# Optimization experiments

Hardware: AMD Instinct MI355X
Metric: run time of the kernel (lower is better)

The kernel has to match this reference:

```python
import jax, jax.numpy as jnp
import numpy as np

B, L, DIM = 4, 2048, 512
H, D = 8, 64
SCALE = D ** -0.5
NEG = -10000.0


def setup_inputs() -> dict:
    key = jax.random.key(0)
    ks = jax.random.split(key, 5)
    std = 1.0 / np.sqrt(DIM)
    return {
        "x": jax.random.normal(ks[0], (B, L, DIM), dtype=jnp.float32),
        "wq": jax.random.normal(ks[1], (H * D, DIM), dtype=jnp.float32) * std,
        "wk": jax.random.normal(ks[2], (H * D, DIM), dtype=jnp.float32) * std,
        "wv": jax.random.normal(ks[3], (H * D, DIM), dtype=jnp.float32) * std,
        "wo": jax.random.normal(ks[4], (DIM, H * D), dtype=jnp.float32) * std,
    }


def reference(x, wq, wk, wv, wo):
    b, l, _ = x.shape
    # projections (torch Linear: y = x @ W.T), split heads -> [b,h,l,d]
    q = (x @ wq.T).reshape(b, l, H, D).transpose(0, 2, 1, 3)
    k = (x @ wk.T).reshape(b, l, H, D).transpose(0, 2, 1, 3)
    v = (x @ wv.T).reshape(b, l, H, D).transpose(0, 2, 1, 3)
    scores = jnp.einsum("bhld,bhsd->bhls", q, k) * SCALE
    scores = jnp.nan_to_num(scores, nan=0.0, posinf=10000.0, neginf=NEG)
    diag = jnp.eye(l, dtype=bool)[None, None]  # [1,1,l,l]
    scores = jnp.where(diag, NEG, scores)
    attn = jax.nn.softmax(scores, axis=-1)
    attn = jnp.where(diag, 0.0, attn)
    attn = jnp.nan_to_num(attn, nan=0.0, posinf=0.0, neginf=0.0)
    out = jnp.einsum("bhls,bhsd->bhld", attn, v)
    out = out.transpose(0, 2, 1, 3).reshape(b, l, H * D)
    return out @ wo.T
```

## Files before the change

kernel.cpp:

```cpp
#include <hip/hip_runtime.h>
#include <hip/hip_bf16.h>


#define Bsz 4
#define Lsz 2048
#define DIMsz 512
#define Hsz 8
#define Dsz 64

typedef _Float16 f16;
typedef __attribute__((ext_vector_type(8))) _Float16 f16x8;
typedef __attribute__((ext_vector_type(4))) _Float16 f16x4;
typedef __attribute__((ext_vector_type(2))) __fp16 fp16x2;
typedef __attribute__((ext_vector_type(4))) float f32x4;
typedef __attribute__((ext_vector_type(16))) float f32x16;
typedef unsigned int u32;
typedef __attribute__((ext_vector_type(2))) unsigned int u32x2;

#if __has_builtin(__builtin_amdgcn_exp2f)
#define EXP2(x) __builtin_amdgcn_exp2f(x)
#else
#define EXP2(x) __expf(0.6931471805599453f * (x))
#endif

__device__ __forceinline__ u32 pack2(float a, float b) {
#if __has_builtin(__builtin_amdgcn_cvt_pkrtz)
    fp16x2 h = __builtin_amdgcn_cvt_pkrtz(a, b);
    return __builtin_bit_cast(u32, h);
#else
    fp16x2 h; h.x = (__fp16)a; h.y = (__fp16)b;
    return __builtin_bit_cast(u32, h);
#endif
}

#if __has_builtin(__builtin_amdgcn_permlane32_swap)
__device__ __forceinline__ void plswap(u32& a, u32& b) {
    u32x2 r = __builtin_amdgcn_permlane32_swap(a, b, false, false);
    a = r.x; b = r.y;
}
#else
__device__ __forceinline__ void plswap(u32& a, u32& b) {
    u32 sa = (u32)__shfl_xor((int)a, 32);
    u32 sb = (u32)__shfl_xor((int)b, 32);
    bool hi = (threadIdx.x & 32) != 0;
    u32 na = hi ? sb : a;
    u32 nb = hi ? b : sa;
    a = na; b = nb;
}
#endif

__device__ __forceinline__ void gl2lds16(const void* g, void* l) {
    __builtin_amdgcn_global_load_lds(
        (const __attribute__((address_space(1))) u32*)g,
        (__attribute__((address_space(3))) u32*)l, 16, 0, 0);
}

__global__ __launch_bounds__(256) void pack_f16(
    const float* __restrict__ x, const float* __restrict__ wq,
    const float* __restrict__ wk, const float* __restrict__ wv,
    const float* __restrict__ wo,
    f16* __restrict__ xh, f16* __restrict__ w3h, f16* __restrict__ woh)
{
    int bx = blockIdx.x, seg, blk;
    if (bx < 4096) { seg = 0; blk = bx; }
    else { seg = 1 + ((bx - 4096) >> 8); blk = (bx - 4096) & 255; }
    const float* s; f16* d; float sc = 1.0f;
    switch (seg) {
        case 0: s = x;  d = xh;            break;
        case 1: s = wq; d = w3h;           sc = 0.18033688011112042f; break;
        case 2: s = wk; d = w3h + 262144;  break;
        case 3: s = wv; d = w3h + 524288;  break;
        default: s = wo; d = woh;          break;
    }
    int i = (blk * 256 + threadIdx.x) * 4;
    float4 v = *(const float4*)(s + i);
    f16x4 o;
    o.x = (f16)(v.x * sc); o.y = (f16)(v.y * sc);
    o.z = (f16)(v.z * sc); o.w = (f16)(v.w * sc);
    *(f16x4*)(d + i) = o;
}

__global__ __launch_bounds__(256) void gemm_qkv_f16(
    const f16* __restrict__ A, const f16* __restrict__ B,
    f16* __restrict__ qh, f16* __restrict__ kh, f16* __restrict__ vth)
{
    __shared__ __align__(16) char smem[32768];
    f16* Ash = (f16*)smem;
    f16* Bsh = (f16*)(smem + 16384);

    const int tid = threadIdx.x;
    const int w = tid >> 6, lane = tid & 63;
    const int quad = lane >> 4, low = lane & 15;
    const int wm = w >> 1, wn = w & 1;
    const int m0 = blockIdx.y * 128, n0 = blockIdx.x * 128;

    f32x4 acc[4][4];
    #pragma unroll
    for (int i = 0; i < 4; i++)
        #pragma unroll
        for (int j = 0; j < 4; j++) acc[i][j] = (f32x4){0.f, 0.f, 0.f, 0.f};

    #pragma unroll 1
    for (int k0 = 0; k0 < DIMsz; k0 += 64) {
        __syncthreads();
        #pragma unroll
        for (int j = 0; j < 4; j++) {
            int t = j * 256 + tid;
            int r = t >> 3, g = t & 7;
            int gc = (g ^ (r & 7)) * 8;
            char* lb = (char*)Ash + (j * 256 + w * 64) * 16;
            gl2lds16(A + (size_t)(m0 + r) * DIMsz + k0 + gc, lb);
            char* lb2 = (char*)Bsh + (j * 256 + w * 64) * 16;
            gl2lds16(B + (size_t)(n0 + r) * DIMsz + k0 + gc, lb2);
        }
        __syncthreads();

        #pragma unroll
        for (int ks2 = 0; ks2 < 2; ks2++) {
            f16x8 af[4], bf[4];
            #pragma unroll
            for (int mt = 0; mt < 4; mt++) {
                int ar = wm * 64 + mt * 16 + low;
                int c = ks2 * 4 + quad;
                af[mt] = *(const f16x8*)&Ash[ar * 64 + ((c ^ (ar & 7)) << 3)];
            }
            #pragma unroll
            for (int nt = 0; nt < 4; nt++) {
                int br = wn * 64 + nt * 16 + low;
                int c = ks2 * 4 + quad;
                bf[nt] = *(const f16x8*)&Bsh[br * 64 + ((c ^ (br & 7)) << 3)];
            }
            #pragma unroll
            for (int mt = 0; mt < 4; mt++)
                #pragma unroll
                for (int nt = 0; nt < 4; nt++)
                    acc[mt][nt] = __builtin_amdgcn_mfma_f32_16x16x32_f16(
                        af[mt], bf[nt], acc[mt][nt], 0, 0, 0);
        }
    }

    const int proj = n0 >> 9;
    if (proj < 2) {
        f16* dst = (proj == 0) ? qh : kh;
        #pragma unroll
        for (int nt = 0; nt < 4; nt++) {
            int n = n0 + wn * 64 + nt * 16 + low;
            int c = n & 511, h = c >> 6, d = c & 63;
            #pragma unroll
            for (int mt = 0; mt < 4; mt++)
                #pragma unroll
                for (int r = 0; r < 4; r++) {
                    int m = m0 + wm * 64 + mt * 16 + quad * 4 + r;
                    int b_ = m >> 11, l = m & (Lsz - 1);
                    size_t bh = (size_t)(b_ * Hsz + h);
                    dst[(bh * Lsz + l) * Dsz + d] = (f16)acc[mt][nt][r];
                }
        }
    } else {
        const int hb = (n0 & 511) >> 6;
        f16* Tv = (f16*)smem;
        const int b_ = m0 >> 11, l0 = m0 & (Lsz - 1);
        #pragma unroll 1
        for (int hs = 0; hs < 2; hs++) {
            __syncthreads();
            if (wn == hs) {
                #pragma unroll
                for (int nt = 0; nt < 4; nt++) {
                    int d = nt * 16 + low;
                    #pragma unroll
                    for (int mt = 0; mt < 4; mt++)
                        #pragma unroll
                        for (int r = 0; r < 4; r++) {
                            int l = wm * 64 + mt * 16 + quad * 4 + r;
                            Tv[d * 136 + l] = (f16)acc[mt][nt][r];
                        }
                }
            }
            __syncthreads();
            int d = tid >> 2, seg = tid & 3;
            size_t bh = (size_t)(b_ * Hsz + hb + hs);
            f16* dstp = vth + (bh * 64 + d) * (size_t)Lsz + l0 + seg * 32;
            const f16* srcp = Tv + d * 136 + seg * 32;
            #pragma unroll
            for (int j = 0; j < 4; j++)
                *(f16x8*)(dstp + j * 8) = *(const f16x8*)(srcp + j * 8);
        }
    }
}

__global__ __launch_bounds__(256, 3) void attn_mfma(
    const f16* __restrict__ q, const f16* __restrict__ k,
    const f16* __restrict__ vt, f16* __restrict__ ctx)
{
    __shared__ __align__(16) char smem[32768];
    __shared__ float Ls[4][2][32];

    f16* Ks = (f16*)smem;
    f16* Vs = (f16*)(smem + 16384);

    const int tid = threadIdx.x;
    const int w = tid >> 6, lane = tid & 63;
    const int col = lane & 31;
    const int h = lane >> 5;
    const int bh = blockIdx.x;
    const int qb = blockIdx.y;
    const int q0 = qb * 64;
    const size_t kvb = (size_t)bh * Lsz;

    f16x8 qf[2][4];
    #pragma unroll
    for (int qt = 0; qt < 2; qt++)
        #pragma unroll
        for (int s = 0; s < 4; s++)
            qf[qt][s] = *(const f16x8*)(q + (kvb + q0 + qt * 32 + col) * Dsz
                                          + s * 16 + h * 8);

    const f16* kp; const f16* vp;
    {
        int rk = tid >> 3, gk = tid & 7;
        kp = k + (kvb + rk) * Dsz + ((gk ^ (rk & 7)) << 3);
        int rv = tid >> 4, gv = tid & 15;
        vp = vt + ((size_t)bh * Dsz + rv) * Lsz + ((gv ^ (rv & 15)) << 3);
    }
    char* kl = (char*)Ks + (w * 64) * 16;
    char* vl = (char*)Vs + (w * 64) * 16;

    const int rk = w * 32 + col;
    const f16* kfp[4];
    #pragma unroll
    for (int s = 0; s < 4; s++)
        kfp[s] = Ks + rk * 64 + (((s * 2 + h) ^ (rk & 7)) << 3);
    const f16* vfp[2][2];
    #pragma unroll
    for (int dt = 0; dt < 2; dt++)
        #pragma unroll
        for (int ks = 0; ks < 2; ks++) {
            int rv = dt * 32 + col, cv = w * 4 + ks * 2 + h;
            vfp[dt][ks] = Vs + rv * 128 + ((cv ^ (rv & 15)) << 3);
        }

    f32x16 acc[2][2];
    #pragma unroll
    for (int qt = 0; qt < 2; qt++)
        #pragma unroll
        for (int dt = 0; dt < 2; dt++)
            #pragma unroll
            for (int i = 0; i < 16; i++) acc[qt][dt][i] = 0.f;
    float lsum[2] = {0.f, 0.f};

    const int drd_s0 = (qb >> 1) * 128;
    const int dqt = w - (qb & 1) * 2;

    #pragma unroll 1
    for (int s0 = 0; s0 < Lsz; s0 += 128) {
        __syncthreads();
        gl2lds16(kp,        kl);
        gl2lds16(kp + 2048, kl + 4096);
        gl2lds16(kp + 4096, kl + 8192);
        gl2lds16(kp + 6144, kl + 12288);
        gl2lds16(vp,            vl);
        gl2lds16(vp + 16 * Lsz, vl + 4096);
        gl2lds16(vp + 32 * Lsz, vl + 8192);
        gl2lds16(vp + 48 * Lsz, vl + 12288);
        kp += 128 * Dsz;
        vp += 128;
        __syncthreads();

        f32x16 st[2];
        #pragma unroll
        for (int i = 0; i < 16; i++) { st[0][i] = 0.f; st[1][i] = 0.f; }
        #pragma unroll
        for (int s = 0; s < 4; s++) {
            f16x8 kf = *(const f16x8*)kfp[s];
            st[0] = __builtin_amdgcn_mfma_f32_32x32x16_f16(kf, qf[0][s], st[0], 0, 0, 0);
            st[1] = __builtin_amdgcn_mfma_f32_32x32x16_f16(kf, qf[1][s], st[1], 0, 0, 0);
        }

        union { u32 u[4]; f16x8 v; } pf[2][2];
        const bool drnd = (s0 == drd_s0);
        #pragma unroll
        for (int qt = 0; qt < 2; qt++) {
            float pv[16];
            #pragma unroll
            for (int i = 0; i < 16; i++) pv[i] = EXP2(st[qt][i]);
            if (drnd && qt == dqt) {
                #pragma unroll
                for (int i = 0; i < 16; i++) {
                    int row = (i & 3) + 8 * (i >> 2) + 4 * h;
                    pv[i] = (row == col) ? 0.f : pv[i];
                }
            }
            #pragma unroll
            for (int i = 0; i < 16; i++) lsum[qt] += pv[i];
            u32 P2[8];
            #pragma unroll
            for (int j = 0; j < 8; j++)
                P2[j] = pack2(pv[2 * j], pv[2 * j + 1]);
            plswap(P2[0], P2[2]); plswap(P2[1], P2[3]);
            plswap(P2[4], P2[6]); plswap(P2[5], P2[7]);
            #pragma unroll
            for (int jj = 0; jj < 4; jj++) {
                pf[qt][0].u[jj] = P2[jj];
                pf[qt][1].u[jj] = P2[4 + jj];
            }
        }

        #pragma unroll
        for (int dt = 0; dt < 2; dt++)
            #pragma unroll
            for (int ks = 0; ks < 2; ks++) {
                f16x8 vf = *(const f16x8*)vfp[dt][ks];
                acc[0][dt] = __builtin_amdgcn_mfma_f32_32x32x16_f16(
                    vf, pf[0][ks].v, acc[0][dt], 0, 0, 0);
                acc[1][dt] = __builtin_amdgcn_mfma_f32_32x32x16_f16(
                    vf, pf[1][ks].v, acc[1][dt], 0, 0, 0);
            }
    }

    #pragma unroll
    for (int qt = 0; qt < 2; qt++) {
        lsum[qt] += __shfl_xor(lsum[qt], 32);
        if (h == 0) Ls[w][qt][col] = lsum[qt];
    }

    float* Om = (float*)smem;
    __syncthreads();
    if (w == 1 || w == 3) {
        float* og = Om + (w >> 1) * 4096;
        #pragma unroll
        for (int qt = 0; qt < 2; qt++)
            #pragma unroll
            for (int dt = 0; dt < 2; dt++)
                #pragma unroll
                for (int i = 0; i < 16; i++) {
                    int row = (i & 3) + 8 * (i >> 2) + 4 * h;
                    og[(dt * 32 + row) * 64 + qt * 32 + col] = acc[qt][dt][i];
                }
    }
    __syncthreads();
    if (w == 0 || w == 2) {
        const float* og = Om + (w >> 1) * 4096;
        #pragma unroll
        for (int qt = 0; qt < 2; qt++)
            #pragma unroll
            for (int dt = 0; dt < 2; dt++)
                #pragma unroll
                for (int i = 0; i < 16; i++) {
                    int row = (i & 3) + 8 * (i >> 2) + 4 * h;
                    acc[qt][dt][i] += og[(dt * 32 + row) * 64 + qt * 32 + col];
                }
    }
    __syncthreads();
    if (w == 2) {
        #pragma unroll
        for (int qt = 0; qt < 2; qt++)
            #pragma unroll
            for (int dt = 0; dt < 2; dt++)
                #pragma unroll
                for (int i = 0; i < 16; i++) {
                    int row = (i & 3) + 8 * (i >> 2) + 4 * h;
                    Om[(dt * 32 + row) * 64 + qt * 32 + col] = acc[qt][dt][i];
                }
    }
    __syncthreads();
    if (w == 0) {
        #pragma unroll
        for (int qt = 0; qt < 2; qt++)
            #pragma unroll
            for (int dt = 0; dt < 2; dt++)
                #pragma unroll
                for (int i = 0; i < 16; i++) {
                    int row = (i & 3) + 8 * (i >> 2) + 4 * h;
                    acc[qt][dt][i] += Om[(dt * 32 + row) * 64 + qt * 32 + col];
                }
        const int b = bh >> 3, hh = bh & 7;
        #pragma unroll
        for (int qt = 0; qt < 2; qt++) {
            float ls = Ls[0][qt][col] + Ls[1][qt][col]
                     + Ls[2][qt][col] + Ls[3][qt][col];
            const float inv = 1.0f / ls;
            f16* op = ctx + ((size_t)(b * Lsz + q0 + qt * 32 + col)) * DIMsz
                          + hh * 64;
            #pragma unroll
            for (int dt = 0; dt < 2; dt++)
                #pragma unroll
                for (int r4 = 0; r4 < 4; r4++) {
                    f16x4 o;
                    o.x = (f16)(acc[qt][dt][4 * r4 + 0] * inv);
                    o.y = (f16)(acc[qt][dt][4 * r4 + 1] * inv);
                    o.z = (f16)(acc[qt][dt][4 * r4 + 2] * inv);
                    o.w = (f16)(acc[qt][dt][4 * r4 + 3] * inv);
                    *(f16x4*)(op + dt * 32 + 8 * r4 + 4 * h) = o;
                }
        }
    }
}

__global__ __launch_bounds__(256) void gemm_out_f16(
    const f16* __restrict__ A, const f16* __restrict__ B,
    float* __restrict__ C)
{
    __shared__ f16 Ash[64 * 64];
    __shared__ f16 Bsh[64 * 64];
    const int tid = threadIdx.x;
    const int w = tid >> 6, lane = tid & 63;
    const int quad = lane >> 4, low = lane & 15;
    const int wm = w >> 1, wn = w & 1;
    const int m0 = blockIdx.y * 64, n0 = blockIdx.x * 64;

    f32x4 acc[2][2];
    #pragma unroll
    for (int i = 0; i < 2; i++)
        #pragma unroll
        for (int j = 0; j < 2; j++) acc[i][j] = (f32x4){0.f, 0.f, 0.f, 0.f};

    #pragma unroll 1
    for (int k0 = 0; k0 < DIMsz; k0 += 64) {
        __syncthreads();
        #pragma unroll
        for (int j = 0; j < 2; j++) {
            int t = j * 256 + tid;
            int r = t >> 3, g = t & 7;
            int gc = (g ^ (r & 7)) * 8;
            char* lb = (char*)Ash + (j * 256 + w * 64) * 16;
            gl2lds16(A + (size_t)(m0 + r) * DIMsz + k0 + gc, lb);
            char* lb2 = (char*)Bsh + (j * 256 + w * 64) * 16;
            gl2lds16(B + (size_t)(n0 + r) * DIMsz + k0 + gc, lb2);
        }
        __syncthreads();

        #pragma unroll
        for (int ks2 = 0; ks2 < 2; ks2++) {
            f16x8 af[2], bf[2];
            #pragma unroll
            for (int mt = 0; mt < 2; mt++) {
                int ar = wm * 32 + mt * 16 + low;
                int c = ks2 * 4 + quad;
                af[mt] = *(const f16x8*)&Ash[ar * 64 + ((c ^ (ar & 7)) << 3)];
            }
            #pragma unroll
            for (int nt = 0; nt < 2; nt++) {
                int br = wn * 32 + nt * 16 + low;
                int c = ks2 * 4 + quad;
                bf[nt] = *(const f16x8*)&Bsh[br * 64 + ((c ^ (br & 7)) << 3)];
            }
            #pragma unroll
            for (int mt = 0; mt < 2; mt++)
                #pragma unroll
                for (int nt = 0; nt < 2; nt++)
                    acc[mt][nt] = __builtin_amdgcn_mfma_f32_16x16x32_f16(
                        af[mt], bf[nt], acc[mt][nt], 0, 0, 0);
        }
    }

    #pragma unroll
    for (int mt = 0; mt < 2; mt++)
        #pragma unroll
        for (int r = 0; r < 4; r++) {
            int m = m0 + wm * 32 + mt * 16 + quad * 4 + r;
            #pragma unroll
            for (int nt = 0; nt < 2; nt++) {
                int n = n0 + wn * 32 + nt * 16 + low;
                C[(size_t)m * DIMsz + n] = acc[mt][nt][r];
            }
        }
}

extern "C" void kernel_launch(void* const* d_in, const int* in_sizes, int n_in,
                              void* d_out, int out_size, void* d_ws, size_t ws_size,
                              hipStream_t stream) {
    const float* x  = (const float*)d_in[0];
    const float* wq = (const float*)d_in[1];
    const float* wk = (const float*)d_in[2];
    const float* wv = (const float*)d_in[3];
    const float* wo = (const float*)d_in[4];
    float* out = (float*)d_out;

    const size_t NTOK = (size_t)Bsz * Lsz;
    const size_t XSZ  = NTOK * DIMsz;

    f16* xh   = (f16*)d_ws;
    f16* w3h  = xh + XSZ;
    f16* woh  = w3h + 3 * 262144;
    f16* qh   = woh + 262144;
    f16* kh   = qh + XSZ;
    f16* vth  = kh + XSZ;
    f16* ctxh = vth + XSZ;

    pack_f16<<<5120, 256, 0, stream>>>(x, wq, wk, wv, wo, xh, w3h, woh);

    dim3 g1(1536 / 128, NTOK / 128);
    gemm_qkv_f16<<<g1, 256, 0, stream>>>(xh, w3h, qh, kh, vth);

    dim3 g2(Bsz * Hsz, Lsz / 64);
    attn_mfma<<<g2, 256, 0, stream>>>(qh, kh, vth, ctxh);

    dim3 g3(DIMsz / 64, NTOK / 64);
    gemm_out_f16<<<g3, 256, 0, stream>>>(ctxh, woh, out);
}
```

Baseline: 165.1 us.

## Double-buffer K/V tiles in LDS with async prefetch and vmcnt waits

Turns the attention loop into a two-stage software pipeline. Shared memory is doubled to 64 KB so the next 128-key K/V tile is loaded directly into LDS while the current tile is being processed. The two __syncthreads per round become explicit vmcnt waits plus raw barriers, and s_setprio raises wave priority around the MFMA sections. The larger LDS footprint cuts the launch bound from 3 to 2 blocks per CU, giving up occupancy in exchange for hiding load latency.

```diff
diff --git a/kernel.cpp b/kernel.cpp
--- a/kernel.cpp
+++ b/kernel.cpp
@@ -188,15 +188,11 @@
     }
 }
 
-__global__ __launch_bounds__(256, 3) void attn_mfma(
+__global__ __launch_bounds__(256, 2) void attn_mfma(
     const f16* __restrict__ q, const f16* __restrict__ k,
     const f16* __restrict__ vt, f16* __restrict__ ctx)
 {
-    __shared__ __align__(16) char smem[32768];
-    __shared__ float Ls[4][2][32];
-
-    f16* Ks = (f16*)smem;
-    f16* Vs = (f16*)(smem + 16384);
+    __shared__ __align__(16) char smem[65536];
 
     const int tid = threadIdx.x;
     const int w = tid >> 6, lane = tid & 63;
@@ -207,6 +203,9 @@
     const int q0 = qb * 64;
     const size_t kvb = (size_t)bh * Lsz;
 
+    f16* Ks = (f16*)smem;
+    f16* Vs = (f16*)(smem + 16384);
+
     f16x8 qf[2][4];
     #pragma unroll
     for (int qt = 0; qt < 2; qt++)
@@ -214,16 +213,21 @@
         for (int s = 0; s < 4; s++)
             qf[qt][s] = *(const f16x8*)(q + (kvb + q0 + qt * 32 + col) * Dsz
                                           + s * 16 + h * 8);
+    #pragma unroll
+    for (int qt = 0; qt < 2; qt++)
+        #pragma unroll
+        for (int s = 0; s < 4; s++)
+            asm volatile("" :: "v"(qf[qt][s]));
 
     const f16* kp; const f16* vp;
     {
-        int rk = tid >> 3, gk = tid & 7;
-        kp = k + (kvb + rk) * Dsz + ((gk ^ (rk & 7)) << 3);
+        int rk_ = tid >> 3, gk = tid & 7;
+        kp = k + (kvb + rk_) * Dsz + ((gk ^ (rk_ & 7)) << 3);
         int rv = tid >> 4, gv = tid & 15;
         vp = vt + ((size_t)bh * Dsz + rv) * Lsz + ((gv ^ (rv & 15)) << 3);
     }
-    char* kl = (char*)Ks + (w * 64) * 16;
-    char* vl = (char*)Vs + (w * 64) * 16;
+    char* kl = (char*)smem + w * 1024;
+    char* vl = (char*)smem + 16384 + w * 1024;
 
     const int rk = w * 32 + col;
     const f16* kfp[4];
@@ -251,76 +255,109 @@
     const int drd_s0 = (qb >> 1) * 128;
     const int dqt = w - (qb & 1) * 2;
 
+    gl2lds16(kp,        kl);
+    gl2lds16(kp + 2048, kl + 4096);
+    gl2lds16(kp + 4096, kl + 8192);
+    gl2lds16(kp + 6144, kl + 12288);
+    gl2lds16(vp,            vl);
+    gl2lds16(vp + 16 * Lsz, vl + 4096);
+    gl2lds16(vp + 32 * Lsz, vl + 8192);
+    gl2lds16(vp + 48 * Lsz, vl + 12288);
+    kp += 128 * Dsz;
+    vp += 128;
+
+#define ATTN_ROUND(S0, P, PRE) do {                                           \
+    const int bufoff_ = (P) * 32768;                                          \
+    if (PRE) {                                                                \
+        const int nx_ = ((P) ^ 1) * 32768;                                    \
+        gl2lds16(kp,        kl + nx_);                                        \
+        gl2lds16(kp + 2048, kl + nx_ + 4096);                                 \
+        gl2lds16(kp + 4096, kl + nx_ + 8192);                                 \
+        gl2lds16(kp + 6144, kl + nx_ + 12288);                                \
+        gl2lds16(vp,            vl + nx_);                                    \
+        gl2lds16(vp + 16 * Lsz, vl + nx_ + 4096);                             \
+        gl2lds16(vp + 32 * Lsz, vl + nx_ + 8192);                             \
+        gl2lds16(vp + 48 * Lsz, vl + nx_ + 12288);                            \
+        kp += 128 * Dsz;                                                      \
+        vp += 128;                                                            \
+        asm volatile("s_waitcnt vmcnt(8)" ::: "memory");                      \
+    } else {                                                                  \
+        asm volatile("s_waitcnt vmcnt(0)" ::: "memory");                      \
+    }                                                                         \
+    __builtin_amdgcn_s_barrier();                                             \
+    __builtin_amdgcn_sched_barrier(0);                                        \
+    \
+    f32x16 st[2];                                                             \
+    _Pragma("unroll")                                                         \
+    for (int i = 0; i < 16; i++) { st[0][i] = 0.f; st[1][i] = 0.f; }          \
+    __builtin_amdgcn_s_setprio(1);                                            \
+    _Pragma("unroll")                                                         \
+    for (int s = 0; s < 4; s++) {                                             \
+        f16x8 kf = *(const f16x8*)((const char*)kfp[s] + bufoff_);            \
+        st[0] = __builtin_amdgcn_mfma_f32_32x32x16_f16(kf, qf[0][s],          \
+                                                       st[0], 0, 0, 0);       \
+        st[1] = __builtin_amdgcn_mfma_f32_32x32x16_f16(kf, qf[1][s],          \
+                                                       st[1], 0, 0, 0);       \
+    }                                                                         \
+    __builtin_amdgcn_s_setprio(0);                                            \
+                \
+    union { u32 u[4]; f16x8 v; } pf[2][2];                                    \
+    const bool drnd_ = ((S0) == drd_s0);                                      \
+    _Pragma("unroll")                                                         \
+    for (int qt = 0; qt < 2; qt++) {                                          \
+        float pv[16];                                                         \
+        _Pragma("unroll")                                                     \
+        for (int i = 0; i < 16; i++) pv[i] = EXP2(st[qt][i]);                 \
+        if (drnd_ && qt == dqt) {                                             \
+            _Pragma("unroll")                                                 \
+            for (int i = 0; i < 16; i++) {                                    \
+                int row = (i & 3) + 8 * (i >> 2) + 4 * h;                     \
+                pv[i] = (row == col) ? 0.f : pv[i];                           \
+            }                                                                 \
+        }                                                                     \
+        _Pragma("unroll")                                                     \
+        for (int i = 0; i < 16; i++) lsum[qt] += pv[i];                       \
+        u32 P2[8];                                                            \
+        _Pragma("unroll")                                                     \
+        for (int j = 0; j < 8; j++)                                           \
+            P2[j] = pack2(pv[2 * j], pv[2 * j + 1]);                          \
+        plswap(P2[0], P2[2]); plswap(P2[1], P2[3]);                           \
+        plswap(P2[4], P2[6]); plswap(P2[5], P2[7]);                           \
+        _Pragma("unroll")                                                     \
+        for (int jj = 0; jj < 4; jj++) {                                      \
+            pf[qt][0].u[jj] = P2[jj];                                         \
+            pf[qt][1].u[jj] = P2[4 + jj];                                     \
+        }                                                                     \
+    }                                                                         \
+    \
+    __builtin_amdgcn_s_setprio(1);                                            \
+    _Pragma("unroll")                                                         \
+    for (int dt = 0; dt < 2; dt++)                                            \
+        _Pragma("unroll")                                                     \
+        for (int ks = 0; ks < 2; ks++) {                                      \
+            f16x8 vf = *(const f16x8*)((const char*)vfp[dt][ks] + bufoff_);   \
+            acc[0][dt] = __builtin_amdgcn_mfma_f32_32x32x16_f16(              \
+                vf, pf[0][ks].v, acc[0][dt], 0, 0, 0);                        \
+            acc[1][dt] = __builtin_amdgcn_mfma_f32_32x32x16_f16(              \
+                vf, pf[1][ks].v, acc[1][dt], 0, 0, 0);                        \
+        }                                                                     \
+    __builtin_amdgcn_s_setprio(0);                                            \
+    __builtin_amdgcn_sched_barrier(0);                                        \
+    __builtin_amdgcn_s_barrier();                                             \
+} while (0)
+
     #pragma unroll 1
-    for (int s0 = 0; s0 < Lsz; s0 += 128) {
-        __syncthreads();
-        gl2lds16(kp,        kl);
-        gl2lds16(kp + 2048, kl + 4096);
-        gl2lds16(kp + 4096, kl + 8192);
-        gl2lds16(kp + 6144, kl + 12288);
-        gl2lds16(vp,            vl);
-        gl2lds16(vp + 16 * Lsz, vl + 4096);
-        gl2lds16(vp + 32 * Lsz, vl + 8192);
-        gl2lds16(vp + 48 * Lsz, vl + 12288);
-        kp += 128 * Dsz;
-        vp += 128;
-        __syncthreads();
-
-        f32x16 st[2];
-        #pragma unroll
-        for (int i = 0; i < 16; i++) { st[0][i] = 0.f; st[1][i] = 0.f; }
-        #pragma unroll
-        for (int s = 0; s < 4; s++) {
-            f16x8 kf = *(const f16x8*)kfp[s];
-            st[0] = __builtin_amdgcn_mfma_f32_32x32x16_f16(kf, qf[0][s], st[0], 0, 0, 0);
-            st[1] = __builtin_amdgcn_mfma_f32_32x32x16_f16(kf, qf[1][s], st[1], 0, 0, 0);
-        }
-
-        union { u32 u[4]; f16x8 v; } pf[2][2];
-        const bool drnd = (s0 == drd_s0);
-        #pragma unroll
-        for (int qt = 0; qt < 2; qt++) {
-            float pv[16];
-            #pragma unroll
-            for (int i = 0; i < 16; i++) pv[i] = EXP2(st[qt][i]);
-            if (drnd && qt == dqt) {
-                #pragma unroll
-                for (int i = 0; i < 16; i++) {
-                    int row = (i & 3) + 8 * (i >> 2) + 4 * h;
-                    pv[i] = (row == col) ? 0.f : pv[i];
-                }
-            }
-            #pragma unroll
-            for (int i = 0; i < 16; i++) lsum[qt] += pv[i];
-            u32 P2[8];
-            #pragma unroll
-            for (int j = 0; j < 8; j++)
-                P2[j] = pack2(pv[2 * j], pv[2 * j + 1]);
-            plswap(P2[0], P2[2]); plswap(P2[1], P2[3]);
-            plswap(P2[4], P2[6]); plswap(P2[5], P2[7]);
-            #pragma unroll
-            for (int jj = 0; jj < 4; jj++) {
-                pf[qt][0].u[jj] = P2[jj];
-                pf[qt][1].u[jj] = P2[4 + jj];
-            }
-        }
-
-        #pragma unroll
-        for (int dt = 0; dt < 2; dt++)
-            #pragma unroll
-            for (int ks = 0; ks < 2; ks++) {
-                f16x8 vf = *(const f16x8*)vfp[dt][ks];
-                acc[0][dt] = __builtin_amdgcn_mfma_f32_32x32x16_f16(
-                    vf, pf[0][ks].v, acc[0][dt], 0, 0, 0);
-                acc[1][dt] = __builtin_amdgcn_mfma_f32_32x32x16_f16(
-                    vf, pf[1][ks].v, acc[1][dt], 0, 0, 0);
-            }
-    }
-
+    for (int s0 = 0; s0 < Lsz; s0 += 256) {
+        ATTN_ROUND(s0, 0, true);
+        ATTN_ROUND(s0 + 128, 1, (s0 + 256 < Lsz));
+    }
+#undef ATTN_ROUND
+
+    float* Lsp = (float*)(smem + 49152);
     #pragma unroll
     for (int qt = 0; qt < 2; qt++) {
         lsum[qt] += __shfl_xor(lsum[qt], 32);
-        if (h == 0) Ls[w][qt][col] = lsum[qt];
+        if (h == 0) Lsp[w * 64 + qt * 32 + col] = lsum[qt];
     }
 
     float* Om = (float*)smem;
@@ -376,8 +413,8 @@
         const int b = bh >> 3, hh = bh & 7;
         #pragma unroll
         for (int qt = 0; qt < 2; qt++) {
-            float ls = Ls[0][qt][col] + Ls[1][qt][col]
-                     + Ls[2][qt][col] + Ls[3][qt][col];
+            float ls = Lsp[qt * 32 + col] + Lsp[64 + qt * 32 + col]
+                     + Lsp[128 + qt * 32 + col] + Lsp[192 + qt * 32 + col];
             const float inv = 1.0f / ls;
             f16* op = ctx + ((size_t)(b * Lsz + q0 + qt * 32 + col)) * DIMsz
                           + hh * 64;
```

New measurement: 165.2 us. No clear change (+0.1%).
